# Optimization experiments

Measured on AMD Instinct MI355X. Metric: run time of the kernel, lower is better.

The kernel has to match this reference:

```python
import jax, jax.numpy as jnp
import numpy as np

FMAPS = 128
B, F, N = 16, 128, 2048


def setup_inputs() -> dict:
    key = jax.random.key(0)
    k1, k2, k3 = jax.random.split(key, 3)
    adj_in = jnp.zeros((B, N, N), dtype=jnp.float32)  # unused by the math (device-check only in torch)
    emb_in = jax.random.normal(k1, (B, F, N), dtype=jnp.float32)
    # parameters, initialized like torch.rand (uniform [0,1))
    v = jax.random.uniform(k2, (FMAPS,), dtype=jnp.float32)
    b = jax.random.uniform(k3, (1,), dtype=jnp.float32)
    return {"adj_in": adj_in, "emb_in": emb_in, "v": v, "b": b}


def reference(adj_in, emb_in, v, b):
    # coord = emb_in / emb_in.std()  (torch std: unbiased over all elements)
    coord = emb_in / jnp.std(emb_in, ddof=1)
    # adj[b,i,j] = sum_f v[f]*(coord[b,f,i] + coord[b,f,j]) + bias
    # = s[b,i] + s[b,j] + bias, where s = v . coord  -> O(B*F*N) instead of per-node bmm loop
    s = jnp.einsum("f,bfn->bn", v, coord)  # [B, N]
    adj = jax.nn.sigmoid(s[:, :, None] + s[:, None, :] + b[0])  # [B, N, N]
    return adj
```

## Files before the change

kernel.cpp:

```cpp
#include <hip/hip_runtime.h>
#include <hip/hip_bf16.h>

#define B_ 16
#define F_ 128
#define N_ 2048
#define M_TOT (B_ * F_ * N_)

__global__ __launch_bounds__(256) void k_reduce(const float* __restrict__ emb,
                                                float* __restrict__ partials) {
    int tid = threadIdx.x;
    int gid = blockIdx.x * blockDim.x + tid;
    int stride = gridDim.x * blockDim.x;

    float s = 0.f, q = 0.f;
    const float4* e4 = (const float4*)emb;
    const int total4 = M_TOT / 4;
    for (int i = gid; i < total4; i += stride) {
        float4 v = e4[i];
        s += v.x + v.y + v.z + v.w;
        q += v.x * v.x + v.y * v.y + v.z * v.z + v.w * v.w;
    }

    #pragma unroll
    for (int off = 32; off > 0; off >>= 1) {
        s += __shfl_down(s, off);
        q += __shfl_down(q, off);
    }

    __shared__ float ls[4], lq[4];
    int wave = tid >> 6;
    if ((tid & 63) == 0) { ls[wave] = s; lq[wave] = q; }
    __syncthreads();
    if (tid == 0) {
        float S = ls[0] + ls[1] + ls[2] + ls[3];
        float Q = lq[0] + lq[1] + lq[2] + lq[3];
        partials[2 * blockIdx.x]     = S;
        partials[2 * blockIdx.x + 1] = Q;
    }
}

__global__ __launch_bounds__(256) void k_finalize(const float* __restrict__ partials,
                                                  float* __restrict__ inv_std,
                                                  int nblk) {
    int tid = threadIdx.x;
    float s = 0.f, q = 0.f;
    for (int i = tid; i < nblk; i += blockDim.x) {
        s += partials[2 * i];
        q += partials[2 * i + 1];
    }
    #pragma unroll
    for (int off = 32; off > 0; off >>= 1) {
        s += __shfl_down(s, off);
        q += __shfl_down(q, off);
    }
    __shared__ float ls[4], lq[4];
    int wave = tid >> 6;
    if ((tid & 63) == 0) { ls[wave] = s; lq[wave] = q; }
    __syncthreads();
    if (tid == 0) {
        float S = ls[0] + ls[1] + ls[2] + ls[3];
        float Q = lq[0] + lq[1] + lq[2] + lq[3];
        float mean = S / (float)M_TOT;
        float var = (Q - S * mean) / (float)(M_TOT - 1);
        inv_std[0] = rsqrtf(var);
    }
}

__global__ __launch_bounds__(256) void k_dot(const float* __restrict__ emb,
                                             const float* __restrict__ v,
                                             const float* __restrict__ bias,
                                             const float* __restrict__ inv_std,
                                             float* __restrict__ t) {
    __shared__ float vs[F_];
    int tid = threadIdx.x;
    if (tid < F_) vs[tid] = v[tid];
    __syncthreads();

    int idx = blockIdx.x * blockDim.x + tid;
    int b = idx >> 11;
    int n = idx & (N_ - 1);
    const float* base = emb + (size_t)b * F_ * N_ + n;

    float acc = 0.f;
    #pragma unroll 8
    for (int f = 0; f < F_; ++f) {
        acc += vs[f] * base[(size_t)f * N_];
    }
    t[idx] = acc * inv_std[0] + 0.5f * bias[0];
}

__device__ __forceinline__ float fast_sigmoid(float x) {
    float e = __expf(-x);
    return __builtin_amdgcn_rcpf(1.0f + e);
}

__global__ __launch_bounds__(256) void k_out(const float* __restrict__ t,
                                             float* __restrict__ out) {
    int row = blockIdx.x;
    int b = row >> 11;
    float si = t[row];

    const float4* t4 = (const float4*)(t + ((size_t)b << 11));
    float4* o4 = (float4*)(out + (size_t)row * N_);

    int tid = threadIdx.x;
    #pragma unroll
    for (int k = 0; k < 2; ++k) {
        int j4 = tid + k * 256;
        float4 tj = t4[j4];
        float4 r;
        r.x = fast_sigmoid(si + tj.x);
        r.y = fast_sigmoid(si + tj.y);
        r.z = fast_sigmoid(si + tj.z);
        r.w = fast_sigmoid(si + tj.w);
        o4[j4] = r;
    }
}

extern "C" void kernel_launch(void* const* d_in, const int* in_sizes, int n_in,
                              void* d_out, int out_size, void* d_ws, size_t ws_size,
                              hipStream_t stream) {
    const float* emb  = (const float*)d_in[1];
    const float* v    = (const float*)d_in[2];
    const float* bias = (const float*)d_in[3];
    float* out = (float*)d_out;

    float* wsf      = (float*)d_ws;
    float* partials = wsf;
    float* inv_std  = wsf + 2048;
    float* t        = wsf + 2304;

    const int RB = 1024;

    k_reduce<<<RB, 256, 0, stream>>>(emb, partials);
    k_finalize<<<1, 256, 0, stream>>>(partials, inv_std, RB);
    k_dot<<<(B_ * N_) / 256, 256, 0, stream>>>(emb, v, bias, inv_std, t);
    k_out<<<B_ * N_, 256, 0, stream>>>(t, out);
}
```

Measured before the change: 400.1 us.

## Fuse std reduction into dot pass and process multiple rows per output block

Computes the sum, sum-of-squares and v-dot in one pass over emb, removing the separate full read for the statistics, and applies the inverse std and half-bias later in the output kernel. The output kernel now handles 16 rows per block, reusing the loaded column vector across rows and writing with nontemporal stores. The cost is fewer blocks in the stats pass (128 instead of 1024 reduction blocks) and strided per-feature loads that carry the statistics work.

```diff
diff --git a/kernel.cpp b/kernel.cpp
--- a/kernel.cpp
+++ b/kernel.cpp
@@ -1,53 +1,36 @@
 #include <hip/hip_runtime.h>
-#include <hip/hip_bf16.h>
 
 #define B_ 16
 #define F_ 128
 #define N_ 2048
 #define M_TOT (B_ * F_ * N_)
 
-__global__ __launch_bounds__(256) void k_reduce(const float* __restrict__ emb,
-                                                float* __restrict__ partials) {
+typedef float f4v __attribute__((ext_vector_type(4)));
+
+__global__ __launch_bounds__(256) void k_stats_dot(const float* __restrict__ emb,
+                                                   const float* __restrict__ v,
+                                                   float* __restrict__ d,
+                                                   float* __restrict__ partials) {
+    __shared__ float vs[F_];
     int tid = threadIdx.x;
-    int gid = blockIdx.x * blockDim.x + tid;
-    int stride = gridDim.x * blockDim.x;
+    if (tid < F_) vs[tid] = v[tid];
+    __syncthreads();
 
-    float s = 0.f, q = 0.f;
-    const float4* e4 = (const float4*)emb;
-    const int total4 = M_TOT / 4;
-    for (int i = gid; i < total4; i += stride) {
-        float4 v = e4[i];
-        s += v.x + v.y + v.z + v.w;
-        q += v.x * v.x + v.y * v.y + v.z * v.z + v.w * v.w;
+    int idx = blockIdx.x * 256 + tid;
+    int b = idx >> 11;
+    int n = idx & (N_ - 1);
+    const float* base = emb + (size_t)b * F_ * N_ + n;
+
+    float acc = 0.f, s = 0.f, q = 0.f;
+    #pragma unroll 8
+    for (int f = 0; f < F_; ++f) {
+        float e = base[(size_t)f * N_];
+        acc += vs[f] * e;
+        s += e;
+        q += e * e;
     }
+    d[idx] = acc;
 
-    #pragma unroll
-    for (int off = 32; off > 0; off >>= 1) {
-        s += __shfl_down(s, off);
-        q += __shfl_down(q, off);
-    }
-
-    __shared__ float ls[4], lq[4];
-    int wave = tid >> 6;
-    if ((tid & 63) == 0) { ls[wave] = s; lq[wave] = q; }
-    __syncthreads();
-    if (tid == 0) {
-        float S = ls[0] + ls[1] + ls[2] + ls[3];
-        float Q = lq[0] + lq[1] + lq[2] + lq[3];
-        partials[2 * blockIdx.x]     = S;
-        partials[2 * blockIdx.x + 1] = Q;
-    }
-}
-
-__global__ __launch_bounds__(256) void k_finalize(const float* __restrict__ partials,
-                                                  float* __restrict__ inv_std,
-                                                  int nblk) {
-    int tid = threadIdx.x;
-    float s = 0.f, q = 0.f;
-    for (int i = tid; i < nblk; i += blockDim.x) {
-        s += partials[2 * i];
-        q += partials[2 * i + 1];
-    }
     #pragma unroll
     for (int off = 32; off > 0; off >>= 1) {
         s += __shfl_down(s, off);
@@ -58,35 +41,38 @@
     if ((tid & 63) == 0) { ls[wave] = s; lq[wave] = q; }
     __syncthreads();
     if (tid == 0) {
-        float S = ls[0] + ls[1] + ls[2] + ls[3];
-        float Q = lq[0] + lq[1] + lq[2] + lq[3];
-        float mean = S / (float)M_TOT;
-        float var = (Q - S * mean) / (float)(M_TOT - 1);
-        inv_std[0] = rsqrtf(var);
+        partials[2 * blockIdx.x]     = ls[0] + ls[1] + ls[2] + ls[3];
+        partials[2 * blockIdx.x + 1] = lq[0] + lq[1] + lq[2] + lq[3];
     }
 }
 
-__global__ __launch_bounds__(256) void k_dot(const float* __restrict__ emb,
-                                             const float* __restrict__ v,
-                                             const float* __restrict__ bias,
-                                             const float* __restrict__ inv_std,
-                                             float* __restrict__ t) {
-    __shared__ float vs[F_];
+__global__ __launch_bounds__(128) void k_finalize(const float* __restrict__ partials,
+                                                  const float* __restrict__ bias,
+                                                  float* __restrict__ scal,
+                                                  int nblk) {
     int tid = threadIdx.x;
-    if (tid < F_) vs[tid] = v[tid];
+    float s = 0.f, q = 0.f;
+    for (int i = tid; i < nblk; i += 128) {
+        s += partials[2 * i];
+        q += partials[2 * i + 1];
+    }
+    #pragma unroll
+    for (int off = 32; off > 0; off >>= 1) {
+        s += __shfl_down(s, off);
+        q += __shfl_down(q, off);
+    }
+    __shared__ float ls[2], lq[2];
+    int wave = tid >> 6;
+    if ((tid & 63) == 0) { ls[wave] = s; lq[wave] = q; }
     __syncthreads();
-
-    int idx = blockIdx.x * blockDim.x + tid;
-    int b = idx >> 11;
-    int n = idx & (N_ - 1);
-    const float* base = emb + (size_t)b * F_ * N_ + n;
-
-    float acc = 0.f;
-    #pragma unroll 8
-    for (int f = 0; f < F_; ++f) {
-        acc += vs[f] * base[(size_t)f * N_];
+    if (tid == 0) {
+        float S = ls[0] + ls[1];
+        float Q = lq[0] + lq[1];
+        float mean = S / (float)M_TOT;
+        float var = (Q - S * mean) / (float)(M_TOT - 1);
+        scal[0] = rsqrtf(var);
+        scal[1] = 0.5f * bias[0];
     }
-    t[idx] = acc * inv_std[0] + 0.5f * bias[0];
 }
 
 __device__ __forceinline__ float fast_sigmoid(float x) {
@@ -94,26 +80,46 @@
     return __builtin_amdgcn_rcpf(1.0f + e);
 }
 
-__global__ __launch_bounds__(256) void k_out(const float* __restrict__ t,
+#define ROWS_PER_BLOCK 16
+
+__global__ __launch_bounds__(256) void k_out(const float* __restrict__ d,
+                                             const float* __restrict__ scal,
                                              float* __restrict__ out) {
-    int row = blockIdx.x;
-    int b = row >> 11;
-    float si = t[row];
+    int tid = threadIdx.x;
+    int b = blockIdx.x >> 7;
+    int i0 = (blockIdx.x & 127) << 4;
+    float inv = scal[0];
+    float hb  = scal[1];
 
-    const float4* t4 = (const float4*)(t + ((size_t)b << 11));
-    float4* o4 = (float4*)(out + (size_t)row * N_);
+    const f4v* d4 = (const f4v*)(d + ((size_t)b << 11));
+    f4v dj0 = d4[tid];
+    f4v dj1 = d4[tid + 256];
+    f4v ej0, ej1;
+    ej0.x = dj0.x * inv + hb;  ej0.y = dj0.y * inv + hb;
+    ej0.z = dj0.z * inv + hb;  ej0.w = dj0.w * inv + hb;
+    ej1.x = dj1.x * inv + hb;  ej1.y = dj1.y * inv + hb;
+    ej1.z = dj1.z * inv + hb;  ej1.w = dj1.w * inv + hb;
 
-    int tid = threadIdx.x;
-    #pragma unroll
-    for (int k = 0; k < 2; ++k) {
-        int j4 = tid + k * 256;
-        float4 tj = t4[j4];
-        float4 r;
-        r.x = fast_sigmoid(si + tj.x);
-        r.y = fast_sigmoid(si + tj.y);
-        r.z = fast_sigmoid(si + tj.z);
-        r.w = fast_sigmoid(si + tj.w);
-        o4[j4] = r;
+    const float* di_row = d + ((size_t)b << 11) + i0;
+
+    #pragma unroll 4
+    for (int r = 0; r < ROWS_PER_BLOCK; ++r) {
+        float ei = di_row[r] * inv + hb;
+        size_t row = ((size_t)b << 11) + (size_t)(i0 + r);
+        f4v* o4 = (f4v*)(out + row * (size_t)N_);
+
+        f4v r0, r1;
+        r0.x = fast_sigmoid(ei + ej0.x);
+        r0.y = fast_sigmoid(ei + ej0.y);
+        r0.z = fast_sigmoid(ei + ej0.z);
+        r0.w = fast_sigmoid(ei + ej0.w);
+        r1.x = fast_sigmoid(ei + ej1.x);
+        r1.y = fast_sigmoid(ei + ej1.y);
+        r1.z = fast_sigmoid(ei + ej1.z);
+        r1.w = fast_sigmoid(ei + ej1.w);
+
+        __builtin_nontemporal_store(r0, o4 + tid);
+        __builtin_nontemporal_store(r1, o4 + tid + 256);
     }
 }
 
@@ -127,13 +133,10 @@
 
     float* wsf      = (float*)d_ws;
     float* partials = wsf;
-    float* inv_std  = wsf + 2048;
-    float* t        = wsf + 2304;
+    float* scal     = wsf + 256;
+    float* dvec     = wsf + 512;
 
-    const int RB = 1024;
-
-    k_reduce<<<RB, 256, 0, stream>>>(emb, partials);
-    k_finalize<<<1, 256, 0, stream>>>(partials, inv_std, RB);
-    k_dot<<<(B_ * N_) / 256, 256, 0, stream>>>(emb, v, bias, inv_std, t);
-    k_out<<<B_ * N_, 256, 0, stream>>>(t, out);
+    k_stats_dot<<<(B_ * N_) / 256, 256, 0, stream>>>(emb, v, dvec, partials);
+    k_finalize<<<1, 128, 0, stream>>>(partials, bias, scal, (B_ * N_) / 256);
+    k_out<<<(B_ * N_) / ROWS_PER_BLOCK, 256, 0, stream>>>(dvec, scal, out);
 }
```

New measurement: 403.0 us. Within noise of the previous version (+0.7%).
